# Optimization experiments

Hardware: AMD Instinct MI355X
Metric: run time of the kernel (lower is better)

Reference implementation:

```python
import jax, jax.numpy as jnp
import numpy as np

N_RBF = 32
R_CUT = 5.0
LAMBDA = 1.0

# real spherical harmonic constants
_C1 = float(np.sqrt(3.0 / (4.0 * np.pi)))            # l=1
_C2A = float(0.5 * np.sqrt(15.0 / np.pi))            # xy, yz, xz
_C2B = float(0.25 * np.sqrt(5.0 / np.pi))            # 3z^2-1
_C2C = float(0.25 * np.sqrt(15.0 / np.pi))           # x^2-y^2


def _sph_l1_l2(u):
    # u: (P,3) unit vectors -> (P, 3+5) real spherical harmonics for l=1,2
    x, y, z = u[:, 0], u[:, 1], u[:, 2]
    l1 = jnp.stack([_C1 * y, _C1 * z, _C1 * x], axis=-1)
    l2 = jnp.stack([
        _C2A * x * y,
        _C2A * y * z,
        _C2B * (3.0 * z * z - 1.0),
        _C2A * x * z,
        _C2C * (x * x - y * y),
    ], axis=-1)
    return jnp.concatenate([l1, l2], axis=-1)


def setup_inputs() -> dict:
    key = jax.random.key(0)
    k1, k2, k3, k4 = jax.random.split(key, 4)
    n, n_pairs = 100000, 3200000
    R = jax.random.normal(k1, (n, 3), dtype=jnp.float32)
    idx_i = jnp.sort(jax.random.randint(k2, (n_pairs,), 0, n, dtype=jnp.int32))
    idx_j = jax.random.randint(k3, (n_pairs,), 0, n, dtype=jnp.int32)
    z = jax.random.randint(k4, (n,), 0, 100, dtype=jnp.int32)
    pair_mask = jnp.ones((n_pairs,), dtype=jnp.float32)
    point_mask = jnp.ones((n,), dtype=jnp.float32)
    return {"R": R, "pair_mask": pair_mask, "point_mask": point_mask,
            "idx_i": idx_i, "idx_j": idx_j, "z": z}


def reference(R, pair_mask, point_mask, idx_i, idx_j, z):
    # gather + displacement, masked (safe_scale)
    r_ij = (R[idx_j] - R[idx_i]) * pair_mask[:, None]          # (P,3)
    # safe norm (avoid NaN grad at r==0)
    sq = jnp.sum(r_ij * r_ij, axis=-1)
    d_ij = jnp.where(sq == 0, 0.0, jnp.sqrt(jnp.where(sq == 0, 1.0, sq)))
    d_ij = d_ij * pair_mask                                    # (P,)

    # gaussian RBF on equidistant centers in [0, r_cut]
    centers = jnp.linspace(0.0, R_CUT, N_RBF, dtype=jnp.float32)
    width = R_CUT / N_RBF
    rbf_ij = jnp.exp(-0.5 * ((d_ij[:, None] - centers) / width) ** 2)
    rbf_ij = rbf_ij * pair_mask[:, None]                       # (P, n_rbf)

    # cosine cutoff
    phi_r_cut = 0.5 * (jnp.cos(jnp.pi * d_ij / R_CUT) + 1.0)
    phi_r_cut = phi_r_cut * (d_ij < R_CUT).astype(d_ij.dtype) * pair_mask

    # safe unit vector (safe_mask)
    denom = jnp.where(d_ij[:, None] == 0, 1.0, d_ij[:, None])
    unit_r_ij = jnp.where(d_ij[:, None] != 0, r_ij / denom, 0.0)
    unit_r_ij = unit_r_ij * pair_mask[:, None]

    # spherical harmonics for degrees [1,2]
    sph_ij = _sph_l1_l2(unit_r_ij) * pair_mask[:, None]        # (P, 8)

    # SPHC: cutoff-weighted scatter-sum per center atom (bincount over idx_i)
    weighted = sph_ij * phi_r_cut[:, None]                     # (P, 8)
    chi = jax.ops.segment_sum(weighted, idx_i, num_segments=R.shape[0])
    chi = chi * point_mask[:, None] / LAMBDA                   # (n, 8)

    return rbf_ij, chi
```

## Files before the change

kernel.cpp:

```cpp
#include <hip/hip_runtime.h>


#define NRBF 32
constexpr float R_CUT   = 5.0f;
constexpr float WIDTH   = R_CUT / NRBF;
constexpr float INV_W   = 1.0f / WIDTH;
constexpr float CSPACE  = R_CUT / (NRBF - 1);
constexpr float PI_F    = 3.14159265358979323846f;
constexpr float LOG2E   = 1.44269504088896340736f;
constexpr float EXP2_A  = -0.5f * LOG2E * INV_W * INV_W;
constexpr float C1  = 0.48860251190291992f;
constexpr float C2A = 1.09254843059207907f;
constexpr float C2B = 0.31539156525252005f;
constexpr float C2C = 0.54627421529603953f;

#define DPP_ROW_SHR(n)  (0x110 + (n))
#define DPP_ROW_BCAST15 0x142
#define DPP_ROW_BCAST31 0x143

typedef float f32x4 __attribute__((ext_vector_type(4)));

template <int CTRL>
__device__ __forceinline__ float fdpp0(float x) {
    return __int_as_float(__builtin_amdgcn_update_dpp(
        0, __float_as_int(x), CTRL, 0xF, 0xF, true));
}

__global__ __launch_bounds__(256) void pack_kernel(
    const float* __restrict__ R, float4* __restrict__ R4, int n)
{
    const int t = blockIdx.x * blockDim.x + threadIdx.x;
    if (t < n) R4[t] = make_float4(R[3*t+0], R[3*t+1], R[3*t+2], 0.0f);
}

template <bool PACKED>
__global__ __launch_bounds__(256) void geom_pairs_kernel(
    const float*  __restrict__ R,
    const float4* __restrict__ R4,
    const float*  __restrict__ pair_mask,
    const float*  __restrict__ point_mask,
    const int*    __restrict__ idx_i,
    const int*    __restrict__ idx_j,
    float* __restrict__ rbf_out,
    float* __restrict__ chi_out,
    int n_pairs)
{
    const int p    = blockIdx.x * blockDim.x + threadIdx.x;
    const int lane = threadIdx.x & 63;

    int   seg  = -1;
    float d_bc = 1e30f;
    float w[8];
    #pragma unroll
    for (int c = 0; c < 8; ++c) w[c] = 0.0f;

    if (p < n_pairs) {
        const int   i = __builtin_nontemporal_load(idx_i + p);
        const int   j = __builtin_nontemporal_load(idx_j + p);
        const float m = __builtin_nontemporal_load(pair_mask + p);
        seg = i;

        float rjx, rjy, rjz, rix, riy, riz;
        if (PACKED) {
            const float4 qj = R4[j];
            const float4 qi = R4[i];
            rjx = qj.x; rjy = qj.y; rjz = qj.z;
            rix = qi.x; riy = qi.y; riz = qi.z;
        } else {
            rjx = R[3*j+0]; rjy = R[3*j+1]; rjz = R[3*j+2];
            rix = R[3*i+0]; riy = R[3*i+1]; riz = R[3*i+2];
        }

        const float rx = (rjx - rix) * m;
        const float ry = (rjy - riy) * m;
        const float rz = (rjz - riz) * m;

        const float sq = rx*rx + ry*ry + rz*rz;
        const float d  = sqrtf(sq) * m;

        d_bc = (m != 0.0f) ? d : 1e30f;

        float phi = 0.5f * (__cosf(PI_F * d * (1.0f/R_CUT)) + 1.0f);
        phi *= (d < R_CUT) ? 1.0f : 0.0f;
        phi *= m;

        const float inv_d = (d != 0.0f) ? (1.0f / d) : 0.0f;
        const float ux = rx * inv_d * m;
        const float uy = ry * inv_d * m;
        const float uz = rz * inv_d * m;

        float s[8];
        s[0] = C1  * uy;
        s[1] = C1  * uz;
        s[2] = C1  * ux;
        s[3] = C2A * ux * uy;
        s[4] = C2A * uy * uz;
        s[5] = C2B * (3.0f * uz * uz - 1.0f) * m;
        s[6] = C2A * ux * uz;
        s[7] = C2C * (ux * ux - uy * uy);

        const float scale = phi * point_mask[i];
        #pragma unroll
        for (int c = 0; c < 8; ++c) w[c] = s[c] * scale;
    }

    {
        const long long wbase = (long long)(p - lane);
        const int sub = lane & 7;
        const int grp = lane >> 3;
        #pragma unroll
        for (int it = 0; it < 8; ++it) {
            const int srcl = it * 8 + grp;
            const float dd = __shfl(d_bc, srcl, 64);
            const long long pr = wbase + srcl;
            if (pr < (long long)n_pairs) {
                const float base = dd - (float)(4 * sub) * CSPACE;
                const float a0 = base;
                const float a1 = base - CSPACE;
                const float a2 = base - 2.0f * CSPACE;
                const float a3 = base - 3.0f * CSPACE;
                f32x4 v;
                v.x = __builtin_amdgcn_exp2f(EXP2_A * a0 * a0);
                v.y = __builtin_amdgcn_exp2f(EXP2_A * a1 * a1);
                v.z = __builtin_amdgcn_exp2f(EXP2_A * a2 * a2);
                v.w = __builtin_amdgcn_exp2f(EXP2_A * a3 * a3);
                __builtin_nontemporal_store(
                    v, (f32x4*)(rbf_out + pr * NRBF + 4 * sub));
            }
        }
    }

    {
        const int prev_seg = __shfl_up(seg, 1, 64);
        const bool head = (lane == 0) || (prev_seg != seg);
        const unsigned long long H = __ballot(head);
        const unsigned long long below = (2ull << lane) - 1ull;
        const int s = 63 - __clzll(H & below);

        {
            const bool ok = (lane - 1) >= s;
            #pragma unroll
            for (int c = 0; c < 8; ++c) { float t = fdpp0<DPP_ROW_SHR(1)>(w[c]); if (ok) w[c] += t; }
        }
        {
            const bool ok = (lane - 2) >= s;
            #pragma unroll
            for (int c = 0; c < 8; ++c) { float t = fdpp0<DPP_ROW_SHR(2)>(w[c]); if (ok) w[c] += t; }
        }
        {
            const bool ok = (lane - 4) >= s;
            #pragma unroll
            for (int c = 0; c < 8; ++c) { float t = fdpp0<DPP_ROW_SHR(4)>(w[c]); if (ok) w[c] += t; }
        }
        {
            const bool ok = (lane - 8) >= s;
            #pragma unroll
            for (int c = 0; c < 8; ++c) { float t = fdpp0<DPP_ROW_SHR(8)>(w[c]); if (ok) w[c] += t; }
        }
        {
            const bool ok = ((lane >> 4) & 1) && (s < (lane & ~15));
            #pragma unroll
            for (int c = 0; c < 8; ++c) { float t = fdpp0<DPP_ROW_BCAST15>(w[c]); if (ok) w[c] += t; }
        }
        {
            const bool ok = (lane >= 32) && (s < 32);
            #pragma unroll
            for (int c = 0; c < 8; ++c) { float t = fdpp0<DPP_ROW_BCAST31>(w[c]); if (ok) w[c] += t; }
        }

        const bool tail = (lane == 63) || (((H >> 1) >> lane) & 1ull);
        if (tail && seg >= 0) {
            float* dst = chi_out + (size_t)seg * 8;
            #pragma unroll
            for (int c = 0; c < 8; ++c) unsafeAtomicAdd(dst + c, w[c]);
        }
    }
}

extern "C" void kernel_launch(void* const* d_in, const int* in_sizes, int n_in,
                              void* d_out, int out_size, void* d_ws, size_t ws_size,
                              hipStream_t stream) {
    const float* R          = (const float*)d_in[0];
    const float* pair_mask  = (const float*)d_in[1];
    const float* point_mask = (const float*)d_in[2];
    const int*   idx_i      = (const int*)d_in[3];
    const int*   idx_j      = (const int*)d_in[4];

    const int n_pairs = in_sizes[1];
    const int n       = in_sizes[2];

    float* rbf_out = (float*)d_out;
    float* chi_out = rbf_out + (size_t)n_pairs * NRBF;

    hipMemsetAsync(chi_out, 0, (size_t)n * 8 * sizeof(float), stream);

    const int block = 256;
    const int grid  = (n_pairs + block - 1) / block;

    const bool packed = (d_ws != nullptr) && (ws_size >= (size_t)n * 16);
    if (packed) {
        float4* R4 = (float4*)d_ws;
        pack_kernel<<<(n + block - 1) / block, block, 0, stream>>>(R, R4, n);
        geom_pairs_kernel<true><<<grid, block, 0, stream>>>(
            R, R4, pair_mask, point_mask, idx_i, idx_j, rbf_out, chi_out, n_pairs);
    } else {
        geom_pairs_kernel<false><<<grid, block, 0, stream>>>(
            R, nullptr, pair_mask, point_mask, idx_i, idx_j, rbf_out, chi_out, n_pairs);
    }
}
```

Measured before the change: 478.1 us.

## Split RBF expansion into a separate streaming kernel via distance buffer

Splits the fused pair kernel in two. The first kernel computes distances, writes them to a workspace array and does the segmented chi scatter. The second kernel streams the RBF output with eight threads per pair. This is meant to decouple the gather- and atomic-heavy work from the large store-bound RBF write, so each kernel gets better occupancy and a simpler memory pattern. The cost is an extra kernel launch plus writing and re-reading the distance array, and the non-packed fallback is dropped, so the code now assumes the workspace is large enough.

Result: slower. 493.5 us (+3.2%).

```diff
diff --git a/kernel.cpp b/kernel.cpp
--- a/kernel.cpp
+++ b/kernel.cpp
@@ -33,23 +33,20 @@
     if (t < n) R4[t] = make_float4(R[3*t+0], R[3*t+1], R[3*t+2], 0.0f);
 }
 
-template <bool PACKED>
-__global__ __launch_bounds__(256) void geom_pairs_kernel(
-    const float*  __restrict__ R,
+__global__ __launch_bounds__(256) void dist_chi_kernel(
     const float4* __restrict__ R4,
     const float*  __restrict__ pair_mask,
     const float*  __restrict__ point_mask,
     const int*    __restrict__ idx_i,
     const int*    __restrict__ idx_j,
-    float* __restrict__ rbf_out,
+    float* __restrict__ d_arr,
     float* __restrict__ chi_out,
     int n_pairs)
 {
     const int p    = blockIdx.x * blockDim.x + threadIdx.x;
     const int lane = threadIdx.x & 63;
 
-    int   seg  = -1;
-    float d_bc = 1e30f;
+    int   seg = -1;
     float w[8];
     #pragma unroll
     for (int c = 0; c < 8; ++c) w[c] = 0.0f;
@@ -60,25 +57,18 @@
         const float m = __builtin_nontemporal_load(pair_mask + p);
         seg = i;
 
-        float rjx, rjy, rjz, rix, riy, riz;
-        if (PACKED) {
-            const float4 qj = R4[j];
-            const float4 qi = R4[i];
-            rjx = qj.x; rjy = qj.y; rjz = qj.z;
-            rix = qi.x; riy = qi.y; riz = qi.z;
-        } else {
-            rjx = R[3*j+0]; rjy = R[3*j+1]; rjz = R[3*j+2];
-            rix = R[3*i+0]; riy = R[3*i+1]; riz = R[3*i+2];
-        }
-
-        const float rx = (rjx - rix) * m;
-        const float ry = (rjy - riy) * m;
-        const float rz = (rjz - riz) * m;
+        const float4 qj = R4[j];
+        const float4 qi = R4[i];
+
+        const float rx = (qj.x - qi.x) * m;
+        const float ry = (qj.y - qi.y) * m;
+        const float rz = (qj.z - qi.z) * m;
 
         const float sq = rx*rx + ry*ry + rz*rz;
         const float d  = sqrtf(sq) * m;
 
-        d_bc = (m != 0.0f) ? d : 1e30f;
+        const float d_bc = (m != 0.0f) ? d : 1e30f;
+        __builtin_nontemporal_store(d_bc, d_arr + p);
 
         float phi = 0.5f * (__cosf(PI_F * d * (1.0f/R_CUT)) + 1.0f);
         phi *= (d < R_CUT) ? 1.0f : 0.0f;
@@ -105,32 +95,6 @@
     }
 
     {
-        const long long wbase = (long long)(p - lane);
-        const int sub = lane & 7;
-        const int grp = lane >> 3;
-        #pragma unroll
-        for (int it = 0; it < 8; ++it) {
-            const int srcl = it * 8 + grp;
-            const float dd = __shfl(d_bc, srcl, 64);
-            const long long pr = wbase + srcl;
-            if (pr < (long long)n_pairs) {
-                const float base = dd - (float)(4 * sub) * CSPACE;
-                const float a0 = base;
-                const float a1 = base - CSPACE;
-                const float a2 = base - 2.0f * CSPACE;
-                const float a3 = base - 3.0f * CSPACE;
-                f32x4 v;
-                v.x = __builtin_amdgcn_exp2f(EXP2_A * a0 * a0);
-                v.y = __builtin_amdgcn_exp2f(EXP2_A * a1 * a1);
-                v.z = __builtin_amdgcn_exp2f(EXP2_A * a2 * a2);
-                v.w = __builtin_amdgcn_exp2f(EXP2_A * a3 * a3);
-                __builtin_nontemporal_store(
-                    v, (f32x4*)(rbf_out + pr * NRBF + 4 * sub));
-            }
-        }
-    }
-
-    {
         const int prev_seg = __shfl_up(seg, 1, 64);
         const bool head = (lane == 0) || (prev_seg != seg);
         const unsigned long long H = __ballot(head);
@@ -175,6 +139,33 @@
             for (int c = 0; c < 8; ++c) unsafeAtomicAdd(dst + c, w[c]);
         }
     }
+}
+
+__global__ __launch_bounds__(256) void rbf_stream_kernel(
+    const float* __restrict__ d_arr,
+    float*       __restrict__ rbf_out,
+    int n_pairs)
+{
+    const int t   = blockIdx.x * blockDim.x + threadIdx.x;
+    const int p   = t >> 3;
+    const int sub = t & 7;
+    if (p >= n_pairs) return;
+
+    const float dd   = d_arr[p];
+    const float base = dd - (float)(4 * sub) * CSPACE;
+    const float a0 = base;
+    const float a1 = base - CSPACE;
+    const float a2 = base - 2.0f * CSPACE;
+    const float a3 = base - 3.0f * CSPACE;
+
+    f32x4 v;
+    v.x = __builtin_amdgcn_exp2f(EXP2_A * a0 * a0);
+    v.y = __builtin_amdgcn_exp2f(EXP2_A * a1 * a1);
+    v.z = __builtin_amdgcn_exp2f(EXP2_A * a2 * a2);
+    v.w = __builtin_amdgcn_exp2f(EXP2_A * a3 * a3);
+
+    __builtin_nontemporal_store(
+        v, (f32x4*)(rbf_out + (size_t)p * NRBF + 4 * sub));
 }
 
 extern "C" void kernel_launch(void* const* d_in, const int* in_sizes, int n_in,
@@ -195,16 +186,18 @@
     hipMemsetAsync(chi_out, 0, (size_t)n * 8 * sizeof(float), stream);
 
     const int block = 256;
-    const int grid  = (n_pairs + block - 1) / block;
-
-    const bool packed = (d_ws != nullptr) && (ws_size >= (size_t)n * 16);
-    if (packed) {
-        float4* R4 = (float4*)d_ws;
-        pack_kernel<<<(n + block - 1) / block, block, 0, stream>>>(R, R4, n);
-        geom_pairs_kernel<true><<<grid, block, 0, stream>>>(
-            R, R4, pair_mask, point_mask, idx_i, idx_j, rbf_out, chi_out, n_pairs);
-    } else {
-        geom_pairs_kernel<false><<<grid, block, 0, stream>>>(
-            R, nullptr, pair_mask, point_mask, idx_i, idx_j, rbf_out, chi_out, n_pairs);
+
+    float4* R4    = (float4*)d_ws;
+    float*  d_arr = (float*)d_ws + (size_t)n * 4;
+
+    pack_kernel<<<(n + block - 1) / block, block, 0, stream>>>(R, R4, n);
+
+    dist_chi_kernel<<<(n_pairs + block - 1) / block, block, 0, stream>>>(
+        R4, pair_mask, point_mask, idx_i, idx_j, d_arr, chi_out, n_pairs);
+
+    {
+        const long long tot = (long long)n_pairs * 8;
+        const int grid = (int)((tot + block - 1) / block);
+        rbf_stream_kernel<<<grid, block, 0, stream>>>(d_arr, rbf_out, n_pairs);
     }
 }
```
